# Kernel tuning notes

Measured on AMD Instinct MI355X. Metric: run time of the kernel, lower is better.

## Reference

```python
import jax, jax.numpy as jnp
import numpy as np

S, N, M = 8, 4096, 64          # snapshots, atoms, total neighbors (sum of max_num_neighs)
L = 20.0                        # periodic box length
R_CS, R_C = 2.0, 6.0            # smooth cutoff radii
DSUB = 16                       # dim_sub_net
PAD_FRAC = 0.15                 # fraction of -1 padded neighbor slots


def _mlp(x, params):
    # DenseChainNet: Linear -> relu between layers, no activation after last layer
    n = len(params)
    for i, (W, b) in enumerate(params):
        x = x @ W + b
        if i < n - 1:
            x = jax.nn.relu(x)
    return x


def _lin(k, fan_in, fan_out):
    k1, k2 = jax.random.split(k)
    s = 1.0 / np.sqrt(fan_in)
    W = jax.random.uniform(k1, (fan_in, fan_out), minval=-s, maxval=s, dtype=jnp.float32)
    b = jax.random.uniform(k2, (fan_out,), minval=-s, maxval=s, dtype=jnp.float32)
    return W, b


def setup_inputs() -> dict:
    key = jax.random.key(0)
    ks = jax.random.split(key, 12)
    inputs = jax.random.uniform(ks[0], (S, N, 3), dtype=jnp.float32) * L
    input_types = jax.random.randint(ks[1], (S, N), 0, 2)
    # neighbor indices, guaranteed != self, with -1 padding
    base = jnp.arange(N, dtype=jnp.int32)[None, :, None]
    off = jax.random.randint(ks[2], (S, N, M), 1, N)
    neigh = (base + off) % N
    pad = jax.random.uniform(ks[3], (S, N, M)) < PAD_FRAC
    neigh_list = jnp.where(pad, -1, neigh).astype(jnp.int32)
    es1_w, es1_b = _lin(ks[4], 2, 4)
    es2_w, es2_b = _lin(ks[5], 4, 4)
    fs1_w, fs1_b = _lin(ks[6], 4, 4)
    fs2_w, fs2_b = _lin(ks[7], 4, 4)
    en1_w, en1_b = _lin(ks[8], 4, 8)
    en2_w, en2_b = _lin(ks[9], 8, 16)
    en3_w, en3_b = _lin(ks[10], 16, 32)
    return dict(inputs=inputs, input_types=input_types, neigh_list=neigh_list,
                es1_w=es1_w, es1_b=es1_b, es2_w=es2_w, es2_b=es2_b,
                fs1_w=fs1_w, fs1_b=fs1_b, fs2_w=fs2_w, fs2_b=fs2_b,
                en1_w=en1_w, en1_b=en1_b, en2_w=en2_w, en2_b=en2_b,
                en3_w=en3_w, en3_b=en3_b)


def reference(inputs, input_types, neigh_list,
              es1_w, es1_b, es2_w, es2_b,
              fs1_w, fs1_b, fs2_w, fs2_b,
              en1_w, en1_b, en2_w, en2_b, en3_w, en3_b):
    mask = neigh_list == -1                               # [S,N,M]
    idx = jnp.where(mask, 0, neigh_list)
    flat = idx.reshape(S, N * M)
    # gather neighbor coordinates with periodic minimum-image convention
    pos_j = jnp.take_along_axis(inputs, flat[..., None], axis=1).reshape(S, N, M, 3)
    d = pos_j - inputs[:, :, None, :]
    d = d - L * jnp.round(d / L)
    r = jnp.sqrt(jnp.sum(d * d, axis=-1) + 1e-12)         # [S,N,M]
    # smooth cutoff: s(r) = 1/r for r<r_cs, cosine switch to 0 at r_c
    u = (r - R_CS) / (R_C - R_CS)
    sw = jnp.where(r < R_CS, 1.0,
                   jnp.where(r < R_C, 0.5 * jnp.cos(jnp.pi * u) + 0.5, 0.0))
    s_ij = jnp.where(mask, 0.0, sw / r)                   # [S,N,M]
    r_ij = d * (s_ij / r)[..., None]                      # s(r) * d / r, [S,N,M,3]
    # species pair descriptor (symmetrized over pair order)
    neigh_types = jnp.take_along_axis(input_types, flat, axis=1).reshape(S, N, M)
    self_t = jnp.broadcast_to(input_types[:, :, None], (S, N, M))
    pairs = jnp.stack([self_t, neigh_types], axis=-1).astype(jnp.float32).reshape(-1, 2)
    es = [(es1_w, es1_b), (es2_w, es2_b)]
    td = _mlp(pairs, es) + _mlp(pairs[:, ::-1], es)
    td = _mlp(td, [(fs1_w, fs1_b), (fs2_w, fs2_b)]).reshape(S, N, M, -1)  # [S,N,M,4]
    s_tilde = (td * s_ij[..., None]).reshape(S * N * M, -1)
    G = _mlp(s_tilde, [(en1_w, en1_b), (en2_w, en2_b), (en3_w, en3_b)]).reshape(S, N, M, -1)  # [S,N,M,32]
    r_tilde = jnp.concatenate([s_ij[..., None], r_ij], axis=-1)            # [S,N,M,4]
    R = jnp.einsum('snmd,snmk->sndk', r_tilde, G[..., :DSUB])              # [S,N,4,16]
    R1 = jnp.einsum('snmd,sndk->snmk', r_tilde, R)                         # [S,N,M,16]
    D = jnp.einsum('snmg,snmk->sngk', G, R1)                               # [S,N,32,16]
    return D
```

## Files before the change

### kernel.cpp

```cpp
#include <hip/hip_runtime.h>
#include <math.h>

#define SS 8
#define NN 4096
#define MM 64
#define LBOX 20.0f

typedef __attribute__((ext_vector_type(8)))  short    short8;
typedef __attribute__((ext_vector_type(4)))  short    s16x4;
typedef __attribute__((ext_vector_type(2)))  float    floatx2;
typedef __attribute__((ext_vector_type(4)))  float    floatx4;
typedef __attribute__((ext_vector_type(2)))  unsigned uintx2;
typedef __attribute__((ext_vector_type(2)))  __bf16   bf16x2;

__device__ inline unsigned pkbf(float a, float b) {
    bf16x2 p; p.x = (__bf16)a; p.y = (__bf16)b;
    unsigned u; __builtin_memcpy(&u, &p, 4); return u;
}

#if defined(__has_builtin)
#  if __has_builtin(__builtin_amdgcn_mfma_f32_16x16x16bf16_1k)
#    define MFMA16(a,b,c) __builtin_amdgcn_mfma_f32_16x16x16bf16_1k(a,b,c,0,0,0)
#  endif
#endif
#ifndef MFMA16
static __device__ inline floatx4 mfma16_asm(s16x4 a, s16x4 b, floatx4 c) {
    floatx4 d;
    asm("v_mfma_f32_16x16x16_bf16 %0, %1, %2, %3\n\ts_nop 7\n\ts_nop 7"
        : "=v"(d) : "v"(a), "v"(b), "v"(c));
    return d;
}
#  define MFMA16(a,b,c) mfma16_asm(a,b,c)
#endif

#define WS_POSW   0
#define WS_WT     (524288 / 4)
#define WT_VT     0
#define WT_B3     32
#define WT_W3F    64

__global__ __launch_bounds__(256) void prep_kernel(
    const float* __restrict__ pos, const int* __restrict__ types,
    const float* __restrict__ es1_w, const float* __restrict__ es1_b,
    const float* __restrict__ es2_w, const float* __restrict__ es2_b,
    const float* __restrict__ fs1_w, const float* __restrict__ fs1_b,
    const float* __restrict__ fs2_w, const float* __restrict__ fs2_b,
    const float* __restrict__ en1_w, const float* __restrict__ en3_w,
    const float* __restrict__ en3_b, float* __restrict__ ws)
{
    const int tid = threadIdx.x;
    const int b = blockIdx.x;
    if (b < 128) {
        const int i = b * 256 + tid;
        floatx4 v;
        v.x = pos[i * 3 + 0];
        v.y = pos[i * 3 + 1];
        v.z = pos[i * 3 + 2];
        v.w = __int_as_float(types[i]);
        *((floatx4*)ws + i) = v;
        return;
    }
    float* wt = ws + WS_WT;
    if (tid < 4) {
        const float ti = (float)(tid >> 1), tj = (float)(tid & 1);
        float e[4] = {0.f, 0.f, 0.f, 0.f};
        #pragma unroll
        for (int swp = 0; swp < 2; ++swp) {
            const float a = swp ? tj : ti, bb = swp ? ti : tj;
            float h[4];
            #pragma unroll
            for (int k = 0; k < 4; ++k)
                h[k] = fmaxf(a * es1_w[k] + bb * es1_w[4 + k] + es1_b[k], 0.f);
            #pragma unroll
            for (int k = 0; k < 4; ++k) {
                float acc = es2_b[k];
                #pragma unroll
                for (int j = 0; j < 4; ++j) acc += h[j] * es2_w[j * 4 + k];
                e[k] += acc;
            }
        }
        float f[4];
        #pragma unroll
        for (int k = 0; k < 4; ++k) {
            float acc = fs1_b[k];
            #pragma unroll
            for (int j = 0; j < 4; ++j) acc += e[j] * fs1_w[j * 4 + k];
            f[k] = fmaxf(acc, 0.f);
        }
        float td[4];
        #pragma unroll
        for (int k = 0; k < 4; ++k) {
            float acc = fs2_b[k];
            #pragma unroll
            for (int j = 0; j < 4; ++j) acc += f[j] * fs2_w[j * 4 + k];
            td[k] = acc;
        }
        #pragma unroll
        for (int o = 0; o < 8; ++o) {
            float acc = 0.f;
            #pragma unroll
            for (int d = 0; d < 4; ++d) acc += td[d] * en1_w[d * 8 + o];
            wt[WT_VT + tid * 8 + o] = acc;
        }
    }
    if (tid < 32)
        wt[WT_B3 + tid] = en3_b[tid];
    if (tid < 128) {
        const int half = tid >> 6, l = tid & 63;
        const int q4 = l >> 4, col = l & 15;
        const int gg = half * 16 + col;
        float v0 = en3_w[(q4 * 4 + 0) * 32 + gg];
        float v1 = en3_w[(q4 * 4 + 1) * 32 + gg];
        float v2 = en3_w[(q4 * 4 + 2) * 32 + gg];
        float v3 = en3_w[(q4 * 4 + 3) * 32 + gg];
        uintx2 pk; pk.x = pkbf(v0, v1); pk.y = pkbf(v2, v3);
        ((uintx2*)(wt + WT_W3F))[tid] = pk;
    }
}

__global__ __launch_bounds__(256) void desc_kernel(
    const float* __restrict__ ws,
    const int*   __restrict__ neigh,
    const float* __restrict__ en1_b,
    const float* __restrict__ en2_w, const float* __restrict__ en2_b,
    float* __restrict__ out)
{
    __shared__ alignas(16) unsigned short sh_h2[4][16][72];
    __shared__ alignas(16) unsigned short sh_rt[4][4][72];
    __shared__ alignas(16) float sh_vt[4][8];
    __shared__ alignas(16) float sh_b3[32];
    __shared__ alignas(16) unsigned sh_w3f[2][64][2];
    __shared__ alignas(16) unsigned short sh_Ab[4][32][4];

    const int tid = threadIdx.x;
    const float* wt = ws + WS_WT;

    if (tid < 32) {
        ((float*)sh_vt)[tid] = wt[WT_VT + tid];
        sh_b3[tid]           = wt[WT_B3 + tid];
    }
    if (tid < 128)
        ((uintx2*)sh_w3f)[tid] = ((const uintx2*)(wt + WT_W3F))[tid];
    __syncthreads();

    const int wave = __builtin_amdgcn_readfirstlane(tid >> 6);
    const int lane = tid & 63;
    const int atom = __builtin_amdgcn_readfirstlane(blockIdx.x * 4 + (tid >> 6));
    const int sbase = atom & ~(NN - 1);
    const floatx4* __restrict__ pw = (const floatx4*)ws;

    const floatx4 pi4 = pw[atom];
    const float xi = pi4.x, yi = pi4.y, zi = pi4.z;
    const int   ti = __float_as_int(pi4.w);

    const int nb  = neigh[atom * MM + lane];
    const int msk = nb < 0;
    const int gj  = sbase + (msk ? 0 : nb);
    const floatx4 pj4 = pw[gj];
    const int tj = __float_as_int(pj4.w);

    float dx = pj4.x - xi;
    float dy = pj4.y - yi;
    float dz = pj4.z - zi;
    dx -= LBOX * rintf(dx * (1.0f / LBOX));
    dy -= LBOX * rintf(dy * (1.0f / LBOX));
    dz -= LBOX * rintf(dz * (1.0f / LBOX));
    const float r2   = fmaf(dx, dx, fmaf(dy, dy, fmaf(dz, dz, 1e-12f)));
    const float rinv = rsqrtf(r2);
    const float r    = r2 * rinv;
    const float u    = fminf(fmaxf((r - 2.0f) * 0.25f, 0.0f), 1.0f);
    const float swv  = 0.5f * __cosf(3.14159265358979323846f * u) + 0.5f;
    const float sij   = msk ? 0.0f : swv * rinv;
    const float scale = sij * rinv;
    const int   tt    = ti * 2 + tj;

    const floatx2 zero2 = {0.f, 0.f};
    const floatx2 sij2  = {sij, sij};
    float h1[8];
    #pragma unroll
    for (int j = 0; j < 4; ++j) {
        const floatx2 vtp = *(const floatx2*)&sh_vt[tt][j * 2];
        const floatx2 ebp = *(const floatx2*)&en1_b[j * 2];
        floatx2 hp = sij2 * vtp + ebp;
        hp = __builtin_elementwise_max(hp, zero2);
        h1[j * 2]     = hp.x;
        h1[j * 2 + 1] = hp.y;
    }

    {
        floatx2 acc[8];
        #pragma unroll
        for (int kp = 0; kp < 8; ++kp)
            acc[kp] = *(const floatx2*)&en2_b[kp * 2];
        #pragma unroll
        for (int i = 0; i < 8; ++i) {
            const floatx2 hi = {h1[i], h1[i]};
            #pragma unroll
            for (int kp = 0; kp < 8; ++kp)
                acc[kp] += hi * (*(const floatx2*)&en2_w[i * 16 + kp * 2]);
        }
        #pragma unroll
        for (int kp = 0; kp < 8; ++kp) {
            const floatx2 a = __builtin_elementwise_max(acc[kp], zero2);
            const unsigned pk = pkbf(a.x, a.y);
            sh_h2[wave][kp * 2][lane]     = (unsigned short)pk;
            sh_h2[wave][kp * 2 + 1][lane] = (unsigned short)(pk >> 16);
        }
    }
    {
        const unsigned p0 = pkbf(sij, dx * scale), p1 = pkbf(dy * scale, dz * scale);
        sh_rt[wave][0][lane] = (unsigned short)p0;
        sh_rt[wave][1][lane] = (unsigned short)(p0 >> 16);
        sh_rt[wave][2][lane] = (unsigned short)p1;
        sh_rt[wave][3][lane] = (unsigned short)(p1 >> 16);
    }
    asm volatile("s_waitcnt lgkmcnt(0)" ::: "memory");

    const int col16 = lane & 15;
    const int q4    = lane >> 4;
    const int m0    = q4 * 8;
    floatx4 cP = {0.f, 0.f, 0.f, 0.f};
    floatx4 cQ = {0.f, 0.f, 0.f, 0.f};
    const short8 ones = (short8)(short)0x3F80;
    #pragma unroll
    for (int ck = 0; ck < 2; ++ck) {
        const short8 af = *(const short8*)&sh_h2[wave][col16][ck * 32 + m0];
        const short8 bf = *(const short8*)&sh_rt[wave][col16 & 3][ck * 32 + m0];
        cP = __builtin_amdgcn_mfma_f32_16x16x32_bf16(af, bf, cP, 0, 0, 0);
        cQ = __builtin_amdgcn_mfma_f32_16x16x32_bf16(ones, bf, cQ, 0, 0, 0);
    }

    s16x4 pfrag;
    {
        const unsigned p0 = pkbf(cP[0], cP[1]), p1 = pkbf(cP[2], cP[3]);
        unsigned* pp = (unsigned*)&pfrag; pp[0] = p0; pp[1] = p1;
    }
    const float qd = cQ[0];
    const s16x4 w3f0 = *(const s16x4*)&sh_w3f[0][lane][0];
    const s16x4 w3f1 = *(const s16x4*)&sh_w3f[1][lane][0];
    const floatx4 b3v0 = *(const floatx4*)&sh_b3[q4 * 4];
    const floatx4 b3v1 = *(const floatx4*)&sh_b3[16 + q4 * 4];
    const floatx4 cA0 = MFMA16(w3f0, pfrag, b3v0 * qd);
    const floatx4 cA1 = MFMA16(w3f1, pfrag, b3v1 * qd);

    if (col16 < 4) {
        #pragma unroll
        for (int j = 0; j < 4; ++j) {
            sh_Ab[wave][q4 * 4 + j][col16]      = (unsigned short)pkbf(cA0[j], 0.f);
            sh_Ab[wave][16 + q4 * 4 + j][col16] = (unsigned short)pkbf(cA1[j], 0.f);
        }
    }
    asm volatile("s_waitcnt lgkmcnt(0)" ::: "memory");
    s16x4 fA0 = *(const s16x4*)&sh_Ab[wave][col16][0];
    s16x4 fA1 = *(const s16x4*)&sh_Ab[wave][16 + col16][0];
    if (q4 != 0) { fA0 = (s16x4)(short)0; fA1 = (s16x4)(short)0; }
    const floatx4 zz = {0.f, 0.f, 0.f, 0.f};
    const floatx4 cD0 = MFMA16(fA0, fA0, zz);
    const floatx4 cD1 = MFMA16(fA1, fA0, zz);

    float* op = out + (size_t)atom * 512;
    #pragma unroll
    for (int j = 0; j < 4; ++j) {
        __builtin_nontemporal_store(cD0[j], op + (q4 * 4 + j) * 16 + col16);
        __builtin_nontemporal_store(cD1[j], op + (16 + 4 * q4 + j) * 16 + col16);
    }
}

extern "C" void kernel_launch(void* const* d_in, const int* in_sizes, int n_in,
                              void* d_out, int out_size, void* d_ws, size_t ws_size,
                              hipStream_t stream) {
    const float* pos   = (const float*)d_in[0];
    const int*   typ   = (const int*)d_in[1];
    const int*   ngh   = (const int*)d_in[2];
    float* ws = (float*)d_ws;

    prep_kernel<<<dim3(129), dim3(256), 0, stream>>>(
        pos, typ,
        (const float*)d_in[3],  (const float*)d_in[4],
        (const float*)d_in[5],  (const float*)d_in[6],
        (const float*)d_in[7],  (const float*)d_in[8],
        (const float*)d_in[9],  (const float*)d_in[10],
        (const float*)d_in[11],
        (const float*)d_in[15], (const float*)d_in[16],
        ws);

    desc_kernel<<<dim3((SS * NN) / 4), dim3(256), 0, stream>>>(
        ws, ngh,
        (const float*)d_in[12],
        (const float*)d_in[13], (const float*)d_in[14],
        (float*)d_out);
}
```

Before: 125.0 us.

## Process four atoms per wave with prefetched neighbor positions

Each wave now loops over four atoms strided by 8192 instead of handling one, and the grid shrinks by four. All neighbor indices are loaded up front, and the next atom's neighbor position gather is issued before the current atom's compute so gather latency overlaps with work. This amortizes the per-block setup (shared weight loads, syncthreads) but cuts block count and parallelism, and the serialized per-iteration LDS waits may limit overlap.

```diff
diff --git a/kernel.cpp b/kernel.cpp
--- a/kernel.cpp
+++ b/kernel.cpp
@@ -145,124 +145,142 @@
 
     const int wave = __builtin_amdgcn_readfirstlane(tid >> 6);
     const int lane = tid & 63;
-    const int atom = __builtin_amdgcn_readfirstlane(blockIdx.x * 4 + (tid >> 6));
-    const int sbase = atom & ~(NN - 1);
+    const int a0   = __builtin_amdgcn_readfirstlane(blockIdx.x * 4 + (tid >> 6));
+    const int sb0  = a0 & ~(NN - 1);
     const floatx4* __restrict__ pw = (const floatx4*)ws;
-
-    const floatx4 pi4 = pw[atom];
-    const float xi = pi4.x, yi = pi4.y, zi = pi4.z;
-    const int   ti = __float_as_int(pi4.w);
-
-    const int nb  = neigh[atom * MM + lane];
-    const int msk = nb < 0;
-    const int gj  = sbase + (msk ? 0 : nb);
-    const floatx4 pj4 = pw[gj];
-    const int tj = __float_as_int(pj4.w);
-
-    float dx = pj4.x - xi;
-    float dy = pj4.y - yi;
-    float dz = pj4.z - zi;
-    dx -= LBOX * rintf(dx * (1.0f / LBOX));
-    dy -= LBOX * rintf(dy * (1.0f / LBOX));
-    dz -= LBOX * rintf(dz * (1.0f / LBOX));
-    const float r2   = fmaf(dx, dx, fmaf(dy, dy, fmaf(dz, dz, 1e-12f)));
-    const float rinv = rsqrtf(r2);
-    const float r    = r2 * rinv;
-    const float u    = fminf(fmaxf((r - 2.0f) * 0.25f, 0.0f), 1.0f);
-    const float swv  = 0.5f * __cosf(3.14159265358979323846f * u) + 0.5f;
-    const float sij   = msk ? 0.0f : swv * rinv;
-    const float scale = sij * rinv;
-    const int   tt    = ti * 2 + tj;
-
-    const floatx2 zero2 = {0.f, 0.f};
-    const floatx2 sij2  = {sij, sij};
-    float h1[8];
-    #pragma unroll
-    for (int j = 0; j < 4; ++j) {
-        const floatx2 vtp = *(const floatx2*)&sh_vt[tt][j * 2];
-        const floatx2 ebp = *(const floatx2*)&en1_b[j * 2];
-        floatx2 hp = sij2 * vtp + ebp;
-        hp = __builtin_elementwise_max(hp, zero2);
-        h1[j * 2]     = hp.x;
-        h1[j * 2 + 1] = hp.y;
-    }
-
-    {
-        floatx2 acc[8];
-        #pragma unroll
-        for (int kp = 0; kp < 8; ++kp)
-            acc[kp] = *(const floatx2*)&en2_b[kp * 2];
-        #pragma unroll
-        for (int i = 0; i < 8; ++i) {
-            const floatx2 hi = {h1[i], h1[i]};
-            #pragma unroll
-            for (int kp = 0; kp < 8; ++kp)
-                acc[kp] += hi * (*(const floatx2*)&en2_w[i * 16 + kp * 2]);
-        }
-        #pragma unroll
-        for (int kp = 0; kp < 8; ++kp) {
-            const floatx2 a = __builtin_elementwise_max(acc[kp], zero2);
-            const unsigned pk = pkbf(a.x, a.y);
-            sh_h2[wave][kp * 2][lane]     = (unsigned short)pk;
-            sh_h2[wave][kp * 2 + 1][lane] = (unsigned short)(pk >> 16);
-        }
-    }
-    {
-        const unsigned p0 = pkbf(sij, dx * scale), p1 = pkbf(dy * scale, dz * scale);
-        sh_rt[wave][0][lane] = (unsigned short)p0;
-        sh_rt[wave][1][lane] = (unsigned short)(p0 >> 16);
-        sh_rt[wave][2][lane] = (unsigned short)p1;
-        sh_rt[wave][3][lane] = (unsigned short)(p1 >> 16);
-    }
-    asm volatile("s_waitcnt lgkmcnt(0)" ::: "memory");
 
     const int col16 = lane & 15;
     const int q4    = lane >> 4;
     const int m0    = q4 * 8;
-    floatx4 cP = {0.f, 0.f, 0.f, 0.f};
-    floatx4 cQ = {0.f, 0.f, 0.f, 0.f};
     const short8 ones = (short8)(short)0x3F80;
+    const floatx2 zero2 = {0.f, 0.f};
+
+    int nbv[4];
     #pragma unroll
-    for (int ck = 0; ck < 2; ++ck) {
-        const short8 af = *(const short8*)&sh_h2[wave][col16][ck * 32 + m0];
-        const short8 bf = *(const short8*)&sh_rt[wave][col16 & 3][ck * 32 + m0];
-        cP = __builtin_amdgcn_mfma_f32_16x16x32_bf16(af, bf, cP, 0, 0, 0);
-        cQ = __builtin_amdgcn_mfma_f32_16x16x32_bf16(ones, bf, cQ, 0, 0, 0);
-    }
-
-    s16x4 pfrag;
+    for (int it = 0; it < 4; ++it)
+        nbv[it] = neigh[(a0 + it * 8192) * MM + lane];
+
+    floatx4 pj_cur;
     {
-        const unsigned p0 = pkbf(cP[0], cP[1]), p1 = pkbf(cP[2], cP[3]);
-        unsigned* pp = (unsigned*)&pfrag; pp[0] = p0; pp[1] = p1;
-    }
-    const float qd = cQ[0];
-    const s16x4 w3f0 = *(const s16x4*)&sh_w3f[0][lane][0];
-    const s16x4 w3f1 = *(const s16x4*)&sh_w3f[1][lane][0];
-    const floatx4 b3v0 = *(const floatx4*)&sh_b3[q4 * 4];
-    const floatx4 b3v1 = *(const floatx4*)&sh_b3[16 + q4 * 4];
-    const floatx4 cA0 = MFMA16(w3f0, pfrag, b3v0 * qd);
-    const floatx4 cA1 = MFMA16(w3f1, pfrag, b3v1 * qd);
-
-    if (col16 < 4) {
+        const int nb = nbv[0];
+        pj_cur = pw[sb0 + (nb < 0 ? 0 : nb)];
+    }
+
+    #pragma unroll
+    for (int it = 0; it < 4; ++it) {
+        const int atom  = a0 + it * 8192;
+        const int msk   = nbv[it] < 0;
+        const floatx4 pj4 = pj_cur;
+        if (it < 3) {
+            const int nbn = nbv[it + 1];
+            pj_cur = pw[sb0 + (it + 1) * 8192 + (nbn < 0 ? 0 : nbn)];
+        }
+        const floatx4 pi4 = pw[atom];
+        const float xi = pi4.x, yi = pi4.y, zi = pi4.z;
+        const int   ti = __float_as_int(pi4.w);
+        const int   tj = __float_as_int(pj4.w);
+
+        float dx = pj4.x - xi;
+        float dy = pj4.y - yi;
+        float dz = pj4.z - zi;
+        dx -= LBOX * rintf(dx * (1.0f / LBOX));
+        dy -= LBOX * rintf(dy * (1.0f / LBOX));
+        dz -= LBOX * rintf(dz * (1.0f / LBOX));
+        const float r2   = fmaf(dx, dx, fmaf(dy, dy, fmaf(dz, dz, 1e-12f)));
+        const float rinv = rsqrtf(r2);
+        const float r    = r2 * rinv;
+        const float u    = fminf(fmaxf((r - 2.0f) * 0.25f, 0.0f), 1.0f);
+        const float swv  = 0.5f * __cosf(3.14159265358979323846f * u) + 0.5f;
+        const float sij   = msk ? 0.0f : swv * rinv;
+        const float scale = sij * rinv;
+        const int   tt    = ti * 2 + tj;
+
+        const floatx2 sij2 = {sij, sij};
+        float h1[8];
         #pragma unroll
         for (int j = 0; j < 4; ++j) {
-            sh_Ab[wave][q4 * 4 + j][col16]      = (unsigned short)pkbf(cA0[j], 0.f);
-            sh_Ab[wave][16 + q4 * 4 + j][col16] = (unsigned short)pkbf(cA1[j], 0.f);
-        }
-    }
-    asm volatile("s_waitcnt lgkmcnt(0)" ::: "memory");
-    s16x4 fA0 = *(const s16x4*)&sh_Ab[wave][col16][0];
-    s16x4 fA1 = *(const s16x4*)&sh_Ab[wave][16 + col16][0];
-    if (q4 != 0) { fA0 = (s16x4)(short)0; fA1 = (s16x4)(short)0; }
-    const floatx4 zz = {0.f, 0.f, 0.f, 0.f};
-    const floatx4 cD0 = MFMA16(fA0, fA0, zz);
-    const floatx4 cD1 = MFMA16(fA1, fA0, zz);
-
-    float* op = out + (size_t)atom * 512;
-    #pragma unroll
-    for (int j = 0; j < 4; ++j) {
-        __builtin_nontemporal_store(cD0[j], op + (q4 * 4 + j) * 16 + col16);
-        __builtin_nontemporal_store(cD1[j], op + (16 + 4 * q4 + j) * 16 + col16);
+            const floatx2 vtp = *(const floatx2*)&sh_vt[tt][j * 2];
+            const floatx2 ebp = *(const floatx2*)&en1_b[j * 2];
+            floatx2 hp = sij2 * vtp + ebp;
+            hp = __builtin_elementwise_max(hp, zero2);
+            h1[j * 2]     = hp.x;
+            h1[j * 2 + 1] = hp.y;
+        }
+
+        {
+            floatx2 acc[8];
+            #pragma unroll
+            for (int kp = 0; kp < 8; ++kp)
+                acc[kp] = *(const floatx2*)&en2_b[kp * 2];
+            #pragma unroll
+            for (int i = 0; i < 8; ++i) {
+                const floatx2 hi = {h1[i], h1[i]};
+                #pragma unroll
+                for (int kp = 0; kp < 8; ++kp)
+                    acc[kp] += hi * (*(const floatx2*)&en2_w[i * 16 + kp * 2]);
+            }
+            #pragma unroll
+            for (int kp = 0; kp < 8; ++kp) {
+                const floatx2 a = __builtin_elementwise_max(acc[kp], zero2);
+                const unsigned pk = pkbf(a.x, a.y);
+                sh_h2[wave][kp * 2][lane]     = (unsigned short)pk;
+                sh_h2[wave][kp * 2 + 1][lane] = (unsigned short)(pk >> 16);
+            }
+        }
+        {
+            const unsigned p0 = pkbf(sij, dx * scale), p1 = pkbf(dy * scale, dz * scale);
+            sh_rt[wave][0][lane] = (unsigned short)p0;
+            sh_rt[wave][1][lane] = (unsigned short)(p0 >> 16);
+            sh_rt[wave][2][lane] = (unsigned short)p1;
+            sh_rt[wave][3][lane] = (unsigned short)(p1 >> 16);
+        }
+        asm volatile("s_waitcnt lgkmcnt(0)" ::: "memory");
+
+        floatx4 cP = {0.f, 0.f, 0.f, 0.f};
+        floatx4 cQ = {0.f, 0.f, 0.f, 0.f};
+        #pragma unroll
+        for (int ck = 0; ck < 2; ++ck) {
+            const short8 af = *(const short8*)&sh_h2[wave][col16][ck * 32 + m0];
+            const short8 bf = *(const short8*)&sh_rt[wave][col16 & 3][ck * 32 + m0];
+            cP = __builtin_amdgcn_mfma_f32_16x16x32_bf16(af, bf, cP, 0, 0, 0);
+            cQ = __builtin_amdgcn_mfma_f32_16x16x32_bf16(ones, bf, cQ, 0, 0, 0);
+        }
+
+        s16x4 pfrag;
+        {
+            const unsigned p0 = pkbf(cP[0], cP[1]), p1 = pkbf(cP[2], cP[3]);
+            unsigned* pp = (unsigned*)&pfrag; pp[0] = p0; pp[1] = p1;
+        }
+        const float qd = cQ[0];
+        const s16x4 w3f0 = *(const s16x4*)&sh_w3f[0][lane][0];
+        const s16x4 w3f1 = *(const s16x4*)&sh_w3f[1][lane][0];
+        const floatx4 b3v0 = *(const floatx4*)&sh_b3[q4 * 4];
+        const floatx4 b3v1 = *(const floatx4*)&sh_b3[16 + q4 * 4];
+        const floatx4 cA0 = MFMA16(w3f0, pfrag, b3v0 * qd);
+        const floatx4 cA1 = MFMA16(w3f1, pfrag, b3v1 * qd);
+
+        if (col16 < 4) {
+            #pragma unroll
+            for (int j = 0; j < 4; ++j) {
+                sh_Ab[wave][q4 * 4 + j][col16]      = (unsigned short)pkbf(cA0[j], 0.f);
+                sh_Ab[wave][16 + q4 * 4 + j][col16] = (unsigned short)pkbf(cA1[j], 0.f);
+            }
+        }
+        asm volatile("s_waitcnt lgkmcnt(0)" ::: "memory");
+        s16x4 fA0 = *(const s16x4*)&sh_Ab[wave][col16][0];
+        s16x4 fA1 = *(const s16x4*)&sh_Ab[wave][16 + col16][0];
+        if (q4 != 0) { fA0 = (s16x4)(short)0; fA1 = (s16x4)(short)0; }
+        const floatx4 zz = {0.f, 0.f, 0.f, 0.f};
+        const floatx4 cD0 = MFMA16(fA0, fA0, zz);
+        const floatx4 cD1 = MFMA16(fA1, fA0, zz);
+
+        float* op = out + (size_t)atom * 512;
+        #pragma unroll
+        for (int j = 0; j < 4; ++j) {
+            __builtin_nontemporal_store(cD0[j], op + (q4 * 4 + j) * 16 + col16);
+            __builtin_nontemporal_store(cD1[j], op + (16 + q4 * 4 + j) * 16 + col16);
+        }
+        asm volatile("s_waitcnt lgkmcnt(0)" ::: "memory");
     }
 }
 
@@ -284,7 +302,7 @@
         (const float*)d_in[15], (const float*)d_in[16],
         ws);
 
-    desc_kernel<<<dim3((SS * NN) / 4), dim3(256), 0, stream>>>(
+    desc_kernel<<<dim3((SS * NN) / 16), dim3(256), 0, stream>>>(
         ws, ngh,
         (const float*)d_in[12],
         (const float*)d_in[13], (const float*)d_in[14],
```

Measured after the change: 124.6 us. No clear change (-0.3%).
